# Kernel tuning notes

Measured on AMD Instinct MI355X. Metric: run time of the kernel, lower is better.

The kernel has to match this reference:

```python
import jax, jax.numpy as jnp
import numpy as np

B, NQ, NK, QS, KS, H, VD = 16, 64, 512, 256, 256, 256, 256


def setup_inputs() -> dict:
    key = jax.random.key(0)
    k1, k2, k3, k4, k5, k6, k7 = jax.random.split(key, 7)
    return {
        "queries": jax.random.normal(k1, (B, NQ, QS), dtype=jnp.float32),
        "keys": jax.random.normal(k2, (B, NK, KS), dtype=jnp.float32),
        "values": jax.random.normal(k3, (B, NK, VD), dtype=jnp.float32),
        "valid_lens": jax.random.randint(k4, (B,), 1, NK + 1, dtype=jnp.int32),
        # learned params (nn.Linear with bias=False): W_q [QS,H], W_k [KS,H], w_v [H]
        "W_q": jax.random.normal(k5, (QS, H), dtype=jnp.float32) / np.sqrt(QS),
        "W_k": jax.random.normal(k6, (KS, H), dtype=jnp.float32) / np.sqrt(KS),
        "w_v": jax.random.normal(k7, (H,), dtype=jnp.float32) / np.sqrt(H),
    }


def reference(queries, keys, values, valid_lens, W_q, W_k, w_v):
    # project: q [B,nq,H], k [B,nk,H]
    q = jnp.einsum("bqd,dh->bqh", queries, W_q)
    k = jnp.einsum("bkd,dh->bkh", keys, W_k)
    # broadcast-add -> tanh -> score reduction via w_v: [B,nq,nk]
    features = jnp.tanh(q[:, :, None, :] + k[:, None, :, :])  # [B,nq,nk,H]
    scores = jnp.einsum("bqkh,h->bqk", features, w_v)
    # masked softmax over keys (positions >= valid_len masked out)
    mask = jnp.arange(scores.shape[-1])[None, None, :] < valid_lens[:, None, None]
    scores = jnp.where(mask, scores, -1e6)
    attn = jax.nn.softmax(scores, axis=-1)
    # weighted sum of values (dropout p=0 / eval mode => identity)
    return jnp.einsum("bqk,bkv->bqv", attn, values)
```

## Files before the change

kernel.cpp:

```cpp
#include <hip/hip_runtime.h>
#include <hip/hip_bf16.h>

#define BB 16
#define NQ 64
#define NK 512
#define HD 256

typedef __attribute__((ext_vector_type(8))) short short8;
typedef __attribute__((ext_vector_type(4))) float f32x4;

__device__ __forceinline__ ushort bf16_rne(float v) {
    unsigned u = __float_as_uint(v);
    return (ushort)((u + 0x7FFFu + ((u >> 16) & 1u)) >> 16);
}
__device__ __forceinline__ float bf16_to_f(ushort h) {
    return __uint_as_float(((unsigned)h) << 16);
}

__global__ __launch_bounds__(256) void convert_split(
    const float* __restrict__ q, const float* __restrict__ k,
    const float* __restrict__ wq, const float* __restrict__ wk,
    ushort* __restrict__ qh, ushort* __restrict__ ql,
    ushort* __restrict__ kh, ushort* __restrict__ kl,
    ushort* __restrict__ wqh, ushort* __restrict__ wql,
    ushort* __restrict__ wkh, ushort* __restrict__ wkl)
{
    const int idx = blockIdx.x * 256 + threadIdx.x;
    if (blockIdx.x < 2304) {
        int e = idx * 4;
        const float* src; ushort *dh, *dl; int off;
        if (e < 1024 * 256) { src = q; dh = qh; dl = ql; off = e; }
        else { src = k; dh = kh; dl = kl; off = e - 1024 * 256; }
        float4 v = *(const float4*)&src[off];
        float fv[4] = {v.x, v.y, v.z, v.w};
        ushort hh[4], ll[4];
        #pragma unroll
        for (int c = 0; c < 4; ++c) {
            hh[c] = bf16_rne(fv[c]);
            ll[c] = bf16_rne(fv[c] - bf16_to_f(hh[c]));
        }
        *(ushort4*)&dh[off] = make_ushort4(hh[0], hh[1], hh[2], hh[3]);
        *(ushort4*)&dl[off] = make_ushort4(ll[0], ll[1], ll[2], ll[3]);
    } else {
        int widx = idx - 2304 * 256;
        const float* W; ushort *wh, *wl;
        if (widx < 16384) { W = wq; wh = wqh; wl = wql; }
        else { W = wk; wh = wkh; wl = wkl; widx -= 16384; }
        int kk = widx >> 6;
        int n4 = (widx & 63) * 4;
        float4 v = *(const float4*)&W[kk * 256 + n4];
        float fv[4] = {v.x, v.y, v.z, v.w};
        #pragma unroll
        for (int c = 0; c < 4; ++c) {
            ushort hh = bf16_rne(fv[c]);
            wh[(n4 + c) * 256 + kk] = hh;
            wl[(n4 + c) * 256 + kk] = bf16_rne(fv[c] - bf16_to_f(hh));
        }
    }
}

__global__ __launch_bounds__(256, 2) void proj_mfma2(
    const ushort* __restrict__ qh, const ushort* __restrict__ ql,
    const ushort* __restrict__ kh, const ushort* __restrict__ kl,
    const ushort* __restrict__ wqh, const ushort* __restrict__ wql,
    const ushort* __restrict__ wkh, const ushort* __restrict__ wkl,
    float* __restrict__ qp, float* __restrict__ kp, float scale)
{
    __shared__ ushort AsH[128 * 64], AsL[128 * 64];
    __shared__ ushort BsH[64 * 64],  BsL[64 * 64];

    const ushort *Ah, *Al, *Bh, *Bl; float* C; int rows0;
    if (blockIdx.x < 8) { Ah = qh; Al = ql; Bh = wqh; Bl = wql; C = qp; rows0 = blockIdx.x * 128; }
    else                { Ah = kh; Al = kl; Bh = wkh; Bl = wkl; C = kp; rows0 = (blockIdx.x - 8) * 128; }
    const int cols0 = blockIdx.y * 64;

    const int t = threadIdx.x, lane = t & 63, wave = t >> 6;
    const int quad = lane >> 4, l15 = lane & 15;
    const int lr = lane >> 3;
    const int cg = (lane & 7) ^ lr;
    const int swz0 = quad ^ (l15 & 7);
    const int swz1 = (quad + 4) ^ (l15 & 7);

    f32x4 acc[2][4];
    #pragma unroll
    for (int i = 0; i < 2; ++i)
        #pragma unroll
        for (int j = 0; j < 4; ++j)
            acc[i][j] = (f32x4){0.f, 0.f, 0.f, 0.f};

    for (int k0 = 0; k0 < 256; k0 += 64) {
        short8 rAh[4], rAl[4], rBh[2], rBl[2];
        #pragma unroll
        for (int i = 0; i < 4; ++i) {
            int ii = wave * 4 + i;
            size_t g = (size_t)(rows0 + ii * 8 + lr) * 256 + k0 + cg * 8;
            rAh[i] = *(const short8*)&Ah[g];
            rAl[i] = *(const short8*)&Al[g];
        }
        #pragma unroll
        for (int j = 0; j < 2; ++j) {
            int jj = wave * 2 + j;
            size_t g = (size_t)(cols0 + jj * 8 + lr) * 256 + k0 + cg * 8;
            rBh[j] = *(const short8*)&Bh[g];
            rBl[j] = *(const short8*)&Bl[g];
        }
        __syncthreads();

        #pragma unroll
        for (int i = 0; i < 4; ++i) {
            int ci = (wave * 4 + i) * 64 + lane;
            *(short8*)&AsH[ci * 8] = rAh[i];
            *(short8*)&AsL[ci * 8] = rAl[i];
        }
        #pragma unroll
        for (int j = 0; j < 2; ++j) {
            int ci = (wave * 2 + j) * 64 + lane;
            *(short8*)&BsH[ci * 8] = rBh[j];
            *(short8*)&BsL[ci * 8] = rBl[j];
        }
        __syncthreads();

        #pragma unroll
        for (int ks = 0; ks < 2; ++ks) {
            const int s = ks ? swz1 : swz0;
            short8 aH[2], aL[2], bH[4], bL[4];
            #pragma unroll
            for (int ms = 0; ms < 2; ++ms) {
                int r = wave * 32 + ms * 16 + l15;
                aH[ms] = *(const short8*)&AsH[r * 64 + s * 8];
                aL[ms] = *(const short8*)&AsL[r * 64 + s * 8];
            }
            #pragma unroll
            for (int ns = 0; ns < 4; ++ns) {
                int n = ns * 16 + l15;
                bH[ns] = *(const short8*)&BsH[n * 64 + s * 8];
                bL[ns] = *(const short8*)&BsL[n * 64 + s * 8];
            }
            #pragma unroll
            for (int ms = 0; ms < 2; ++ms)
                #pragma unroll
                for (int ns = 0; ns < 4; ++ns) {
                    acc[ms][ns] = __builtin_amdgcn_mfma_f32_16x16x32_bf16(aH[ms], bH[ns], acc[ms][ns], 0, 0, 0);
                    acc[ms][ns] = __builtin_amdgcn_mfma_f32_16x16x32_bf16(aL[ms], bH[ns], acc[ms][ns], 0, 0, 0);
                    acc[ms][ns] = __builtin_amdgcn_mfma_f32_16x16x32_bf16(aH[ms], bL[ns], acc[ms][ns], 0, 0, 0);
                }
        }
    }

    #pragma unroll
    for (int ms = 0; ms < 2; ++ms) {
        int rbase = rows0 + wave * 32 + ms * 16 + quad * 4;
        #pragma unroll
        for (int ns = 0; ns < 4; ++ns) {
            int col = cols0 + ns * 16 + l15;
            #pragma unroll
            for (int r = 0; r < 4; ++r)
                C[(size_t)(rbase + r) * 256 + col] = acc[ms][ns][r] * scale;
        }
    }
}

__global__ __launch_bounds__(256, 2) void attn_kernel(
    const float* __restrict__ qp,
    const float* __restrict__ kp,
    const float* __restrict__ values,
    const int*   __restrict__ vlens,
    const float* __restrict__ w_v,
    float* __restrict__ out)
{
    __shared__ float q_s[2][HD];
    __shared__ float wv_s[HD];
    __shared__ float sc[2][NK];
    __shared__ float part[4][2][HD];
    __shared__ float redm[4], reds[4], invs[2];

    const int b     = blockIdx.x & 15;
    const int qpair = blockIdx.x >> 4;
    const int qi0   = qpair * 2;
    const int t     = threadIdx.x;
    const int lane  = t & 63;
    const int wave  = t >> 6;
    const int vl    = vlens[b];
    const size_t row0 = (size_t)b * NQ + qi0;

    q_s[0][t] = qp[row0 * HD + t];
    q_s[1][t] = qp[(row0 + 1) * HD + t];
    wv_s[t]   = w_v[t];
    __syncthreads();

    float Wsum;
    {
        float ws = wv_s[lane] + wv_s[lane + 64] + wv_s[lane + 128] + wv_s[lane + 192];
        #pragma unroll
        for (int off = 32; off; off >>= 1) ws += __shfl_xor(ws, off);
        Wsum = ws;
    }

    const int keyLoc = lane >> 4;
    const int ch     = lane & 15;
    float4 qa[4], qb[4], wf[4];
    #pragma unroll
    for (int m = 0; m < 4; ++m) {
        qa[m] = *(const float4*)&q_s[0][ch * 4 + m * 64];
        qb[m] = *(const float4*)&q_s[1][ch * 4 + m * 64];
        wf[m] = *(const float4*)&wv_s[ch * 4 + m * 64];
    }

    const float* kbase = kp + (size_t)b * NK * HD;
    const int n0 = wave * 4 + keyLoc;
    const float* kptr = kbase + (size_t)n0 * HD + ch * 4;

    float4 kk[4];
    if (n0 < vl) {
        #pragma unroll
        for (int m = 0; m < 4; ++m) kk[m] = *(const float4*)(kptr + m * 64);
    }

    for (int nBase = wave * 4; nBase < vl; nBase += 16) {
        const int nn = nBase + keyLoc;
        float4 kn[4];
        if (nn + 16 < vl) {
            #pragma unroll
            for (int m = 0; m < 4; ++m) kn[m] = *(const float4*)(kptr + 16 * HD + m * 64);
        }
        float p0 = 0.f, p1 = 0.f;
        if (nn < vl) {
            #pragma unroll
            for (int m = 0; m < 4; ++m) {
                float kv[4] = {kk[m].x, kk[m].y, kk[m].z, kk[m].w};
                float qav[4] = {qa[m].x, qa[m].y, qa[m].z, qa[m].w};
                float qbv[4] = {qb[m].x, qb[m].y, qb[m].z, qb[m].w};
                float wv4[4] = {wf[m].x, wf[m].y, wf[m].z, wf[m].w};
                #pragma unroll
                for (int c = 0; c < 4; ++c) {
                    float r0 = __builtin_amdgcn_rcpf(__builtin_amdgcn_exp2f(qav[c] + kv[c]) + 1.f);
                    float r1 = __builtin_amdgcn_rcpf(__builtin_amdgcn_exp2f(qbv[c] + kv[c]) + 1.f);
                    p0 = fmaf(wv4[c], r0, p0);
                    p1 = fmaf(wv4[c], r1, p1);
                }
            }
        }
        p0 += __shfl_down(p0, 8); p0 += __shfl_down(p0, 4);
        p0 += __shfl_down(p0, 2); p0 += __shfl_down(p0, 1);
        p1 += __shfl_down(p1, 8); p1 += __shfl_down(p1, 4);
        p1 += __shfl_down(p1, 2); p1 += __shfl_down(p1, 1);
        if (ch == 0 && nn < vl) {
            sc[0][nn] = fmaf(-2.f, p0, Wsum);
            sc[1][nn] = fmaf(-2.f, p1, Wsum);
        }
        #pragma unroll
        for (int m = 0; m < 4; ++m) kk[m] = kn[m];
        kptr += 16 * HD;
    }
    __syncthreads();

    const int vla = (vl + 15) & ~15;
    {
        const int qq  = wave >> 1;
        const int sub = wave & 1;
        float m = -1e30f;
        for (int n = sub * 64 + lane; n < vl; n += 128) m = fmaxf(m, sc[qq][n]);
        #pragma unroll
        for (int off = 32; off; off >>= 1) m = fmaxf(m, __shfl_xor(m, off));
        if (lane == 0) redm[wave] = m;
        __syncthreads();
        m = fmaxf(redm[qq * 2], redm[qq * 2 + 1]);

        float ssum = 0.f;
        const float L2E = 1.4426950408889634f;
        for (int n = sub * 64 + lane; n < vl; n += 128) {
            float p = __builtin_amdgcn_exp2f((sc[qq][n] - m) * L2E);
            sc[qq][n] = p;
            ssum += p;
        }
        #pragma unroll
        for (int off = 32; off; off >>= 1) ssum += __shfl_xor(ssum, off);
        if (lane == 0) reds[wave] = ssum;
        if (vl + t < vla) { sc[0][vl + t] = 0.f; sc[1][vl + t] = 0.f; }
        __syncthreads();
        if (t == 0)  invs[0] = __builtin_amdgcn_rcpf(reds[0] + reds[1]);
        if (t == 64) invs[1] = __builtin_amdgcn_rcpf(reds[2] + reds[3]);
    }
    __syncthreads();

    float4 acc0 = {0.f, 0.f, 0.f, 0.f};
    float4 acc1 = {0.f, 0.f, 0.f, 0.f};
    const float* vbase = values + (size_t)b * NK * HD;
    for (int nb = wave * 4; nb < vla; nb += 16) {
        float4 v[4]; float pa[4], pb[4];
        #pragma unroll
        for (int u = 0; u < 4; ++u) {
            v[u]  = *(const float4*)&vbase[(size_t)(nb + u) * HD + lane * 4];
            pa[u] = sc[0][nb + u];
            pb[u] = sc[1][nb + u];
        }
        #pragma unroll
        for (int u = 0; u < 4; ++u) {
            acc0.x = fmaf(pa[u], v[u].x, acc0.x);
            acc0.y = fmaf(pa[u], v[u].y, acc0.y);
            acc0.z = fmaf(pa[u], v[u].z, acc0.z);
            acc0.w = fmaf(pa[u], v[u].w, acc0.w);
            acc1.x = fmaf(pb[u], v[u].x, acc1.x);
            acc1.y = fmaf(pb[u], v[u].y, acc1.y);
            acc1.z = fmaf(pb[u], v[u].z, acc1.z);
            acc1.w = fmaf(pb[u], v[u].w, acc1.w);
        }
    }
    *(float4*)&part[wave][0][lane * 4] = acc0;
    *(float4*)&part[wave][1][lane * 4] = acc1;
    __syncthreads();

    if (wave < 2) {
        float4 p0 = *(const float4*)&part[0][wave][lane * 4];
        float4 p1 = *(const float4*)&part[1][wave][lane * 4];
        float4 p2 = *(const float4*)&part[2][wave][lane * 4];
        float4 p3 = *(const float4*)&part[3][wave][lane * 4];
        const float inv = invs[wave];
        float4 o;
        o.x = ((p0.x + p1.x) + (p2.x + p3.x)) * inv;
        o.y = ((p0.y + p1.y) + (p2.y + p3.y)) * inv;
        o.z = ((p0.z + p1.z) + (p2.z + p3.z)) * inv;
        o.w = ((p0.w + p1.w) + (p2.w + p3.w)) * inv;
        *(float4*)&out[(row0 + wave) * HD + lane * 4] = o;
    }
}

extern "C" void kernel_launch(void* const* d_in, const int* in_sizes, int n_in,
                              void* d_out, int out_size, void* d_ws, size_t ws_size,
                              hipStream_t stream) {
    const float* queries = (const float*)d_in[0];
    const float* keys    = (const float*)d_in[1];
    const float* values  = (const float*)d_in[2];
    const int*   vlens   = (const int*)d_in[3];
    const float* W_q     = (const float*)d_in[4];
    const float* W_k     = (const float*)d_in[5];
    const float* w_v     = (const float*)d_in[6];
    float* out = (float*)d_out;

    float*  kp  = (float*)d_ws;
    ushort* qh  = (ushort*)((char*)d_ws + (8 << 20));
    ushort* ql  = qh  + 1024 * 256;
    ushort* kh  = ql  + 1024 * 256;
    ushort* kl  = kh  + 8192 * 256;
    ushort* wqh = kl  + 8192 * 256;
    ushort* wql = wqh + 65536;
    ushort* wkh = wql + 65536;
    ushort* wkl = wkh + 65536;

    float* qp = out;

    const float SC = 2.885390081777927f;

    convert_split<<<dim3(2432), 256, 0, stream>>>(queries, keys, W_q, W_k,
                                                  qh, ql, kh, kl,
                                                  wqh, wql, wkh, wkl);
    proj_mfma2<<<dim3(72, 4), 256, 0, stream>>>(qh, ql, kh, kl,
                                                wqh, wql, wkh, wkl,
                                                qp, kp, SC);
    attn_kernel<<<dim3(512), 256, 0, stream>>>(qp, kp, values, vlens, w_v, out);
}
```

Baseline: 123.5 us.

## Prefetch next K-tile in projection GEMM and remove per-key branches in attention

```diff
diff --git a/kernel.cpp b/kernel.cpp
--- a/kernel.cpp
+++ b/kernel.cpp
@@ -46,16 +46,17 @@
         const float* W; ushort *wh, *wl;
         if (widx < 16384) { W = wq; wh = wqh; wl = wql; }
         else { W = wk; wh = wkh; wl = wkl; widx -= 16384; }
-        int kk = widx >> 6;
-        int n4 = (widx & 63) * 4;
-        float4 v = *(const float4*)&W[kk * 256 + n4];
-        float fv[4] = {v.x, v.y, v.z, v.w};
+        int n  = widx >> 6;
+        int k4 = (widx & 63) * 4;
+        ushort hh[4], ll[4];
         #pragma unroll
         for (int c = 0; c < 4; ++c) {
-            ushort hh = bf16_rne(fv[c]);
-            wh[(n4 + c) * 256 + kk] = hh;
-            wl[(n4 + c) * 256 + kk] = bf16_rne(fv[c] - bf16_to_f(hh));
-        }
+            float v = W[(k4 + c) * 256 + n];
+            hh[c] = bf16_rne(v);
+            ll[c] = bf16_rne(v - bf16_to_f(hh[c]));
+        }
+        *(ushort4*)&wh[n * 256 + k4] = make_ushort4(hh[0], hh[1], hh[2], hh[3]);
+        *(ushort4*)&wl[n * 256 + k4] = make_ushort4(ll[0], ll[1], ll[2], ll[3]);
     }
 }
 
@@ -88,24 +89,22 @@
         for (int j = 0; j < 4; ++j)
             acc[i][j] = (f32x4){0.f, 0.f, 0.f, 0.f};
 
+    short8 rAh[4], rAl[4], rBh[2], rBl[2];
+    #pragma unroll
+    for (int i = 0; i < 4; ++i) {
+        size_t g = (size_t)(rows0 + (wave * 4 + i) * 8 + lr) * 256 + cg * 8;
+        rAh[i] = *(const short8*)&Ah[g];
+        rAl[i] = *(const short8*)&Al[g];
+    }
+    #pragma unroll
+    for (int j = 0; j < 2; ++j) {
+        size_t g = (size_t)(cols0 + (wave * 2 + j) * 8 + lr) * 256 + cg * 8;
+        rBh[j] = *(const short8*)&Bh[g];
+        rBl[j] = *(const short8*)&Bl[g];
+    }
+
     for (int k0 = 0; k0 < 256; k0 += 64) {
-        short8 rAh[4], rAl[4], rBh[2], rBl[2];
-        #pragma unroll
-        for (int i = 0; i < 4; ++i) {
-            int ii = wave * 4 + i;
-            size_t g = (size_t)(rows0 + ii * 8 + lr) * 256 + k0 + cg * 8;
-            rAh[i] = *(const short8*)&Ah[g];
-            rAl[i] = *(const short8*)&Al[g];
-        }
-        #pragma unroll
-        for (int j = 0; j < 2; ++j) {
-            int jj = wave * 2 + j;
-            size_t g = (size_t)(cols0 + jj * 8 + lr) * 256 + k0 + cg * 8;
-            rBh[j] = *(const short8*)&Bh[g];
-            rBl[j] = *(const short8*)&Bl[g];
-        }
         __syncthreads();
-
         #pragma unroll
         for (int i = 0; i < 4; ++i) {
             int ci = (wave * 4 + i) * 64 + lane;
@@ -120,6 +119,21 @@
         }
         __syncthreads();
 
+        if (k0 + 64 < 256) {
+            #pragma unroll
+            for (int i = 0; i < 4; ++i) {
+                size_t g = (size_t)(rows0 + (wave * 4 + i) * 8 + lr) * 256 + k0 + 64 + cg * 8;
+                rAh[i] = *(const short8*)&Ah[g];
+                rAl[i] = *(const short8*)&Al[g];
+            }
+            #pragma unroll
+            for (int j = 0; j < 2; ++j) {
+                size_t g = (size_t)(cols0 + (wave * 2 + j) * 8 + lr) * 256 + k0 + 64 + cg * 8;
+                rBh[j] = *(const short8*)&Bh[g];
+                rBl[j] = *(const short8*)&Bl[g];
+            }
+        }
+
         #pragma unroll
         for (int ks = 0; ks < 2; ++ks) {
             const int s = ks ? swz1 : swz0;
@@ -139,11 +153,18 @@
             #pragma unroll
             for (int ms = 0; ms < 2; ++ms)
                 #pragma unroll
-                for (int ns = 0; ns < 4; ++ns) {
+                for (int ns = 0; ns < 4; ++ns)
                     acc[ms][ns] = __builtin_amdgcn_mfma_f32_16x16x32_bf16(aH[ms], bH[ns], acc[ms][ns], 0, 0, 0);
+            #pragma unroll
+            for (int ms = 0; ms < 2; ++ms)
+                #pragma unroll
+                for (int ns = 0; ns < 4; ++ns)
                     acc[ms][ns] = __builtin_amdgcn_mfma_f32_16x16x32_bf16(aL[ms], bH[ns], acc[ms][ns], 0, 0, 0);
+            #pragma unroll
+            for (int ms = 0; ms < 2; ++ms)
+                #pragma unroll
+                for (int ns = 0; ns < 4; ++ns)
                     acc[ms][ns] = __builtin_amdgcn_mfma_f32_16x16x32_bf16(aH[ms], bL[ns], acc[ms][ns], 0, 0, 0);
-                }
         }
     }
 
@@ -181,6 +202,7 @@
     const int lane  = t & 63;
     const int wave  = t >> 6;
     const int vl    = vlens[b];
+    const int vla   = (vl + 15) & ~15;
     const size_t row0 = (size_t)b * NQ + qi0;
 
     q_s[0][t] = qp[row0 * HD + t];
@@ -207,46 +229,39 @@
     }
 
     const float* kbase = kp + (size_t)b * NK * HD;
-    const int n0 = wave * 4 + keyLoc;
-    const float* kptr = kbase + (size_t)n0 * HD + ch * 4;
+    const float* kptr  = kbase + (size_t)(wave * 4 + keyLoc) * HD + ch * 4;
 
     float4 kk[4];
-    if (n0 < vl) {
-        #pragma unroll
-        for (int m = 0; m < 4; ++m) kk[m] = *(const float4*)(kptr + m * 64);
-    }
-
-    for (int nBase = wave * 4; nBase < vl; nBase += 16) {
-        const int nn = nBase + keyLoc;
+    #pragma unroll
+    for (int m = 0; m < 4; ++m) kk[m] = *(const float4*)(kptr + m * 64);
+
+    for (int nb = wave * 4; nb < vla; nb += 16) {
         float4 kn[4];
-        if (nn + 16 < vl) {
-            #pragma unroll
-            for (int m = 0; m < 4; ++m) kn[m] = *(const float4*)(kptr + 16 * HD + m * 64);
-        }
+        #pragma unroll
+        for (int m = 0; m < 4; ++m) kn[m] = *(const float4*)(kptr + 16 * HD + m * 64);
+
         float p0 = 0.f, p1 = 0.f;
-        if (nn < vl) {
-            #pragma unroll
-            for (int m = 0; m < 4; ++m) {
-                float kv[4] = {kk[m].x, kk[m].y, kk[m].z, kk[m].w};
-                float qav[4] = {qa[m].x, qa[m].y, qa[m].z, qa[m].w};
-                float qbv[4] = {qb[m].x, qb[m].y, qb[m].z, qb[m].w};
-                float wv4[4] = {wf[m].x, wf[m].y, wf[m].z, wf[m].w};
-                #pragma unroll
-                for (int c = 0; c < 4; ++c) {
-                    float r0 = __builtin_amdgcn_rcpf(__builtin_amdgcn_exp2f(qav[c] + kv[c]) + 1.f);
-                    float r1 = __builtin_amdgcn_rcpf(__builtin_amdgcn_exp2f(qbv[c] + kv[c]) + 1.f);
-                    p0 = fmaf(wv4[c], r0, p0);
-                    p1 = fmaf(wv4[c], r1, p1);
-                }
+        #pragma unroll
+        for (int m = 0; m < 4; ++m) {
+            float kv[4]  = {kk[m].x, kk[m].y, kk[m].z, kk[m].w};
+            float qav[4] = {qa[m].x, qa[m].y, qa[m].z, qa[m].w};
+            float qbv[4] = {qb[m].x, qb[m].y, qb[m].z, qb[m].w};
+            float wv4[4] = {wf[m].x, wf[m].y, wf[m].z, wf[m].w};
+            #pragma unroll
+            for (int c = 0; c < 4; ++c) {
+                float r0 = __builtin_amdgcn_rcpf(__builtin_amdgcn_exp2f(qav[c] + kv[c]) + 1.f);
+                float r1 = __builtin_amdgcn_rcpf(__builtin_amdgcn_exp2f(qbv[c] + kv[c]) + 1.f);
+                p0 = fmaf(wv4[c], r0, p0);
+                p1 = fmaf(wv4[c], r1, p1);
             }
         }
         p0 += __shfl_down(p0, 8); p0 += __shfl_down(p0, 4);
         p0 += __shfl_down(p0, 2); p0 += __shfl_down(p0, 1);
         p1 += __shfl_down(p1, 8); p1 += __shfl_down(p1, 4);
         p1 += __shfl_down(p1, 2); p1 += __shfl_down(p1, 1);
-        if (ch == 0 && nn < vl) {
-            sc[0][nn] = fmaf(-2.f, p0, Wsum);
-            sc[1][nn] = fmaf(-2.f, p1, Wsum);
+        if (ch == 0) {
+            sc[0][nb + keyLoc] = fmaf(-2.f, p0, Wsum);
+            sc[1][nb + keyLoc] = fmaf(-2.f, p1, Wsum);
         }
         #pragma unroll
         for (int m = 0; m < 4; ++m) kk[m] = kn[m];
@@ -254,7 +269,6 @@
     }
     __syncthreads();
 
-    const int vla = (vl + 15) & ~15;
     {
         const int qq  = wave >> 1;
         const int sub = wave & 1;
```

Result: faster. 119.6 us (-3.2%).
